# Performance work log

Measured on AMD Instinct MI355X. Metric: run time of the kernel, lower is better.

Reference implementation:

```python
import jax, jax.numpy as jnp
import numpy as np
import math

B, S, DM, DQ, DK, DV = 4, 4096, 512, 512, 512, 512
MASKED = True


def setup_inputs() -> dict:
    key = jax.random.key(0)
    ks = jax.random.split(key, 9)
    s = 1.0 / math.sqrt(DM)  # ~ torch Linear init scale
    return {
        "q_in": jax.random.normal(ks[0], (B, S, DM), jnp.float32),
        "k_in": jax.random.normal(ks[1], (B, S, DM), jnp.float32),
        "v_in": jax.random.normal(ks[2], (B, S, DM), jnp.float32),
        "Wq": jax.random.uniform(ks[3], (DQ, DM), jnp.float32, -s, s),
        "bq": jax.random.uniform(ks[4], (DQ,), jnp.float32, -s, s),
        "Wk": jax.random.uniform(ks[5], (DK, DM), jnp.float32, -s, s),
        "bk": jax.random.uniform(ks[6], (DK,), jnp.float32, -s, s),
        "Wv": jax.random.uniform(ks[7], (DV, DM), jnp.float32, -s, s),
        "bv": jax.random.uniform(ks[8], (DV,), jnp.float32, -s, s),
    }


def reference(q_in, k_in, v_in, Wq, bq, Wk, bk, Wv, bv):
    # Linear projections (torch Linear: x @ W.T + b)
    q = jnp.einsum("bsm,qm->bsq", q_in, Wq) + bq  # [B,S,DQ]
    k = jnp.einsum("bsm,km->bsk", k_in, Wk) + bk  # [B,S,DK]
    v = jnp.einsum("bsm,vm->bsv", v_in, Wv) + bv  # [B,S,DV]

    scale = 1.0 / math.sqrt(k.shape[-1])
    scores = jnp.einsum("bqd,bkd->bqk", q, k) * scale  # [B,S,S]
    if MASKED:
        # Faithful to torch.tril on the scores: upper triangle set to 0 (NOT -inf)
        tri = jnp.tril(jnp.ones((scores.shape[1], scores.shape[2]), bool))
        scores = jnp.where(tri, scores, jnp.zeros((), scores.dtype))
    attn = jax.nn.softmax(scores, axis=-1)
    return jnp.einsum("bqk,bkv->bqv", attn, v)  # [B,S,DV]
```

## Files before the change

### kernel.cpp

```cpp
#include <hip/hip_runtime.h>

typedef unsigned short u16;
typedef unsigned int   u32;
typedef __bf16  bf16x8 __attribute__((ext_vector_type(8)));
typedef u16     u16x8  __attribute__((ext_vector_type(8)));
typedef float   f32x4  __attribute__((ext_vector_type(4)));

#define S_LEN   4096
#define DMODEL  512
#define NBATCH  4
#define NTILE   32
#define NPAIR   528

__device__ __forceinline__ u16 f2bf(float x){
  u32 u = __float_as_uint(x);
  return (u16)((u + 0x7fffu + ((u >> 16) & 1u)) >> 16);
}
__device__ __forceinline__ float bf2f(u16 u){ return __uint_as_float(((u32)u) << 16); }

__device__ __forceinline__ void gload_lds16(const void* g, void* l){
  __builtin_amdgcn_global_load_lds((const __attribute__((address_space(1))) void*)g,
                                   (__attribute__((address_space(3))) void*)l, 16, 0, 0);
}

__device__ __forceinline__ bf16x8 ones_frag(){
  u16x8 u = {0x3F80,0x3F80,0x3F80,0x3F80,0x3F80,0x3F80,0x3F80,0x3F80};
  return __builtin_bit_cast(bf16x8, u);
}

__global__ __launch_bounds__(256) void cast_kernel(const float* __restrict__ in,
                                                   u16* __restrict__ out, int n8){
  int i = blockIdx.x * 256 + threadIdx.x;
  int stride = gridDim.x * 256;
  for (; i < n8; i += stride){
    const float4* p = (const float4*)in + (size_t)i * 2;
    float4 a = p[0], b = p[1];
    ushort4 o0 = make_ushort4(f2bf(a.x), f2bf(a.y), f2bf(a.z), f2bf(a.w));
    ushort4 o1 = make_ushort4(f2bf(b.x), f2bf(b.y), f2bf(b.z), f2bf(b.w));
    ((ushort4*)out)[(size_t)i*2]   = o0;
    ((ushort4*)out)[(size_t)i*2+1] = o1;
  }
}

template<bool ZS>
__device__ __forceinline__ void mma_step(const u16* __restrict__ A, int lda,
                                         const u16* __restrict__ B, int ldb,
                                         u16* ldsA, u16* ldsB,
                                         f32x4 acc[4][4], f32x4* accz, bf16x8 ones,
                                         int w, int l, int wr, int wc)
{
  int srow = l >> 2, scol = (l & 3) * 8;
  #pragma unroll
  for (int cc = 0; cc < 2; ++cc){
    int c = w + cc * 4;
    gload_lds16(A + (size_t)(c*16 + srow)*lda + scol, ldsA + c*512);
    gload_lds16(B + (size_t)(c*16 + srow)*ldb + scol, ldsB + c*512);
  }
  __syncthreads();
  int lo = l & 15, hi = l >> 4;
  bf16x8 a[4], b[4];
  #pragma unroll
  for (int m = 0; m < 4; m++) a[m] = *(const bf16x8*)(ldsA + (wr*64 + m*16 + lo)*32 + hi*8);
  #pragma unroll
  for (int n = 0; n < 4; n++) b[n] = *(const bf16x8*)(ldsB + (wc*64 + n*16 + lo)*32 + hi*8);
  #pragma unroll
  for (int m = 0; m < 4; m++){
    if constexpr (ZS)
      accz[m] = __builtin_amdgcn_mfma_f32_16x16x32_bf16(a[m], ones, accz[m], 0, 0, 0);
    #pragma unroll
    for (int n = 0; n < 4; n++)
      acc[m][n] = __builtin_amdgcn_mfma_f32_16x16x32_bf16(a[m], b[n], acc[m][n], 0, 0, 0);
  }
  __syncthreads();
}

__global__ __launch_bounds__(256) void proj_kernel(const u16* __restrict__ X,
                                                   const u16* __restrict__ W,
                                                   const float* __restrict__ bias,
                                                   u16* __restrict__ Y)
{
  __shared__ __align__(16) u16 ldsA[4096], ldsB[4096];
  int cn = blockIdx.x, rm = blockIdx.y;
  int t = threadIdx.x, w = t >> 6, l = t & 63, wr = w >> 1, wc = w & 1;
  f32x4 zero = {0.f,0.f,0.f,0.f};
  f32x4 acc[4][4];
  #pragma unroll
  for (int m = 0; m < 4; m++)
    #pragma unroll
    for (int n = 0; n < 4; n++) acc[m][n] = zero;

  const u16* A = X + (size_t)rm * 128 * DMODEL;
  const u16* B = W + (size_t)cn * 128 * DMODEL;
  for (int s = 0; s < 16; s++)
    mma_step<false>(A + s*32, DMODEL, B + s*32, DMODEL, ldsA, ldsB, acc, nullptr,
                    ones_frag(), w, l, wr, wc);

  int lo = l & 15, hi = l >> 4;
  #pragma unroll
  for (int n = 0; n < 4; n++){
    int col = cn*128 + wc*64 + n*16 + lo;
    float bs = bias[col];
    #pragma unroll
    for (int m = 0; m < 4; m++){
      int row0 = rm*128 + wr*64 + m*16 + hi*4;
      #pragma unroll
      for (int j = 0; j < 4; j++)
        Y[(size_t)(row0 + j) * DMODEL + col] = f2bf(acc[m][n][j] + bs);
    }
  }
}

__global__ __launch_bounds__(256) void transpose_kernel(const u16* __restrict__ V,
                                                        u16* __restrict__ Vt)
{
  __shared__ u16 tile[64][66];
  int k0 = blockIdx.x * 64, c0 = blockIdx.y * 64, b = blockIdx.z;
  int t = threadIdx.x;
  #pragma unroll
  for (int i = 0; i < 16; i++){
    int idx = i*256 + t; int r = idx >> 6, c = idx & 63;
    tile[r][c] = V[((size_t)b*S_LEN + k0 + r) * DMODEL + c0 + c];
  }
  __syncthreads();
  #pragma unroll
  for (int i = 0; i < 16; i++){
    int idx = i*256 + t; int r = idx >> 6, c = idx & 63;
    Vt[((size_t)b*DMODEL + c0 + r) * S_LEN + k0 + c] = tile[c][r];
  }
}

__global__ __launch_bounds__(256) void vpart_kernel(const u16* __restrict__ V,
                                                    float* __restrict__ part){
  int t = blockIdx.x, b = blockIdx.y, c = threadIdx.x;
  const u16* base = V + ((size_t)b*S_LEN + t*128) * DMODEL;
  float s0 = 0.f, s1 = 0.f;
  for (int k = 0; k < 128; k++){
    s0 += bf2f(base[(size_t)k*DMODEL + c]);
    s1 += bf2f(base[(size_t)k*DMODEL + 256 + c]);
  }
  part[((size_t)b*NTILE + t)*DMODEL + c]       = s0;
  part[((size_t)b*NTILE + t)*DMODEL + 256 + c] = s1;
}

__global__ void suffix_kernel(const float* __restrict__ part, float* __restrict__ sufx){
  int b = blockIdx.x, c = threadIdx.x;
  float s = 0.f;
  for (int t = NTILE - 1; t >= 0; t--){
    sufx[((size_t)b*NTILE + t)*DMODEL + c] = s;
    s += part[((size_t)b*NTILE + t)*DMODEL + c];
  }
}

__global__ __launch_bounds__(256) void score_kernel(const u16* __restrict__ Q,
                                                    const u16* __restrict__ K,
                                                    u16* __restrict__ P)
{
  __shared__ __align__(16) u16 ldsA[4096], ldsB[4096];
  int p = blockIdx.x, b = blockIdx.y;
  int qt = (int)((sqrtf(8.f*p + 1.f) - 1.f) * 0.5f);
  while ((qt+1)*(qt+2)/2 <= p) qt++;
  while (qt*(qt+1)/2 > p) qt--;
  int kt = p - qt*(qt+1)/2;

  int t = threadIdx.x, w = t >> 6, l = t & 63, wr = w >> 1, wc = w & 1;
  f32x4 zero = {0.f,0.f,0.f,0.f};
  f32x4 acc[4][4];
  #pragma unroll
  for (int m = 0; m < 4; m++)
    #pragma unroll
    for (int n = 0; n < 4; n++) acc[m][n] = zero;

  const u16* A = Q + ((size_t)b*S_LEN + qt*128) * DMODEL;
  const u16* B = K + ((size_t)b*S_LEN + kt*128) * DMODEL;
  for (int s = 0; s < 16; s++)
    mma_step<false>(A + s*32, DMODEL, B + s*32, DMODEL, ldsA, ldsB, acc, nullptr,
                    ones_frag(), w, l, wr, wc);

  const float scale = 0.044194173824159216f;
  u16* Pt = P + ((size_t)b*NPAIR + p) * 16384;
  int lo = l & 15, hi = l >> 4;
  bool diag = (qt == kt);
  #pragma unroll
  for (int m = 0; m < 4; m++){
    #pragma unroll
    for (int n = 0; n < 4; n++){
      int cl = wc*64 + n*16 + lo;
      #pragma unroll
      for (int j = 0; j < 4; j++){
        int rl = wr*64 + m*16 + hi*4 + j;
        float s = acc[m][n][j] * scale;
        if (diag && cl > rl) s = 0.f;
        Pt[(size_t)rl*128 + cl] = f2bf(__expf(s));
      }
    }
  }
}

__global__ __launch_bounds__(256) void pv_kernel(const u16* __restrict__ P,
                                                 const u16* __restrict__ Vt,
                                                 const float* __restrict__ sufx,
                                                 float* __restrict__ out)
{
  __shared__ __align__(16) u16 ldsA[4096], ldsB[4096];
  int ct = blockIdx.x, qt = (NTILE - 1) - blockIdx.y, b = blockIdx.z;
  int t = threadIdx.x, w = t >> 6, l = t & 63, wr = w >> 1, wc = w & 1;
  f32x4 zero = {0.f,0.f,0.f,0.f};
  f32x4 acc[4][4]; f32x4 accz[4];
  #pragma unroll
  for (int m = 0; m < 4; m++){
    accz[m] = zero;
    #pragma unroll
    for (int n = 0; n < 4; n++) acc[m][n] = zero;
  }
  bf16x8 ones = ones_frag();

  for (int kt = 0; kt <= qt; ++kt){
    const u16* A = P + ((size_t)b*NPAIR + qt*(qt+1)/2 + kt) * 16384;
    const u16* B = Vt + ((size_t)b*DMODEL + ct*128) * S_LEN + kt*128;
    #pragma unroll 1
    for (int s = 0; s < 4; s++)
      mma_step<true>(A + s*32, 128, B + s*32, S_LEN, ldsA, ldsB, acc, accz,
                     ones, w, l, wr, wc);
  }

  float zadd = (float)(S_LEN - (qt+1)*128);
  int lo = l & 15, hi = l >> 4;
  const float* suf = sufx + ((size_t)b*NTILE + qt)*DMODEL + ct*128;
  #pragma unroll
  for (int m = 0; m < 4; m++){
    #pragma unroll
    for (int j = 0; j < 4; j++){
      float Z = accz[m][j] + zadd;
      int rl = wr*64 + m*16 + hi*4 + j;
      #pragma unroll
      for (int n = 0; n < 4; n++){
        int cl = wc*64 + n*16 + lo;
        float o = (acc[m][n][j] + suf[cl]) / Z;
        out[((size_t)b*S_LEN + qt*128 + rl) * DMODEL + ct*128 + cl] = o;
      }
    }
  }
}

extern "C" void kernel_launch(void* const* d_in, const int* in_sizes, int n_in,
                              void* d_out, int out_size, void* d_ws, size_t ws_size,
                              hipStream_t stream)
{
  const float* q_in = (const float*)d_in[0];
  const float* k_in = (const float*)d_in[1];
  const float* v_in = (const float*)d_in[2];
  const float* Wq   = (const float*)d_in[3];
  const float* bq   = (const float*)d_in[4];
  const float* Wk   = (const float*)d_in[5];
  const float* bk   = (const float*)d_in[6];
  const float* Wv   = (const float*)d_in[7];
  const float* bv   = (const float*)d_in[8];
  float* out = (float*)d_out;
  char*  ws  = (char*)d_ws;

  const size_t NTOK  = (size_t)NBATCH * S_LEN;
  const size_t TEN_B = NTOK * DMODEL * 2;

  size_t off = 0;
  u16* Wq_b = (u16*)(ws + off); off += DMODEL*DMODEL*2;
  u16* Wk_b = (u16*)(ws + off); off += DMODEL*DMODEL*2;
  u16* Wv_b = (u16*)(ws + off); off += DMODEL*DMODEL*2;
  size_t uoff = off;
  u16* qx = (u16*)(ws + uoff);
  u16* kx = qx + NTOK*DMODEL;
  u16* vx = kx + NTOK*DMODEL;
  u16* Pbuf = (u16*)(ws + uoff);
  size_t usize = (size_t)NBATCH * NPAIR * 16384 * 2;
  off = uoff + usize;
  u16* Qb  = (u16*)(ws + off); off += TEN_B;
  u16* Kb  = (u16*)(ws + off); off += TEN_B;
  u16* Vb  = (u16*)(ws + off); off += TEN_B;
  u16* Vtb = (u16*)(ws + off); off += TEN_B;
  float* part = (float*)(ws + off); off += (size_t)NBATCH*NTILE*DMODEL*4;
  float* sufx = (float*)(ws + off); off += (size_t)NBATCH*NTILE*DMODEL*4;

  int n8_big = (int)(NTOK * DMODEL / 8);
  int n8_w   = DMODEL * DMODEL / 8;
  cast_kernel<<<2048, 256, 0, stream>>>(q_in, qx, n8_big);
  cast_kernel<<<2048, 256, 0, stream>>>(k_in, kx, n8_big);
  cast_kernel<<<2048, 256, 0, stream>>>(v_in, vx, n8_big);
  cast_kernel<<<128, 256, 0, stream>>>(Wq, Wq_b, n8_w);
  cast_kernel<<<128, 256, 0, stream>>>(Wk, Wk_b, n8_w);
  cast_kernel<<<128, 256, 0, stream>>>(Wv, Wv_b, n8_w);

  dim3 pg(DMODEL/128, (unsigned)(NTOK/128));
  proj_kernel<<<pg, 256, 0, stream>>>(qx, Wq_b, bq, Qb);
  proj_kernel<<<pg, 256, 0, stream>>>(kx, Wk_b, bk, Kb);
  proj_kernel<<<pg, 256, 0, stream>>>(vx, Wv_b, bv, Vb);

  transpose_kernel<<<dim3(S_LEN/64, DMODEL/64, NBATCH), 256, 0, stream>>>(Vb, Vtb);
  vpart_kernel<<<dim3(NTILE, NBATCH), 256, 0, stream>>>(Vb, part);
  suffix_kernel<<<NBATCH, DMODEL, 0, stream>>>(part, sufx);

  score_kernel<<<dim3(NPAIR, NBATCH), 256, 0, stream>>>(Qb, Kb, Pbuf);
  pv_kernel<<<dim3(DMODEL/128, NTILE, NBATCH), 256, 0, stream>>>(Pbuf, Vtb, sufx, out);
}
```

Before: 379.0 us.

## Retile score and PV kernels to single-wave 64x64 tiles with double-buffered LDS

Score and PV kernels move from 256-thread 128x128 tiles to 64-thread 64x64 tiles. Each uses a double-buffered LDS pipeline with explicit waitcnt, and block indices are remapped for XCD-aware scheduling. The softmax denominator is now built in the score kernel with shuffle reductions and atomics, which removes the extra ones-MFMA from PV. The three cast launches and the three projection launches are each merged into one grid. The smaller tiles give more blocks and better balance on the causal triangle, but each block gets less data reuse, and the atomics and a zeroing launch add overhead.

```diff
diff --git a/kernel.cpp b/kernel.cpp
--- a/kernel.cpp
+++ b/kernel.cpp
@@ -11,6 +11,7 @@
 #define NBATCH  4
 #define NTILE   32
 #define NPAIR   528
+#define SCALE   0.044194173824159216f
 
 __device__ __forceinline__ u16 f2bf(float x){
   u32 u = __float_as_uint(x);
@@ -23,79 +24,76 @@
                                    (__attribute__((address_space(3))) void*)l, 16, 0, 0);
 }
 
-__device__ __forceinline__ bf16x8 ones_frag(){
-  u16x8 u = {0x3F80,0x3F80,0x3F80,0x3F80,0x3F80,0x3F80,0x3F80,0x3F80};
-  return __builtin_bit_cast(bf16x8, u);
-}
-
-__global__ __launch_bounds__(256) void cast_kernel(const float* __restrict__ in,
-                                                   u16* __restrict__ out, int n8){
+__global__ __launch_bounds__(256) void cast3_kernel(const float* __restrict__ a,
+                                                    const float* __restrict__ b,
+                                                    const float* __restrict__ c,
+                                                    u16* oa, u16* ob, u16* oc, int n8){
+  int z = blockIdx.y;
+  const float* in = (z == 0) ? a : (z == 1) ? b : c;
+  u16* out = (z == 0) ? oa : (z == 1) ? ob : oc;
   int i = blockIdx.x * 256 + threadIdx.x;
   int stride = gridDim.x * 256;
   for (; i < n8; i += stride){
     const float4* p = (const float4*)in + (size_t)i * 2;
-    float4 a = p[0], b = p[1];
-    ushort4 o0 = make_ushort4(f2bf(a.x), f2bf(a.y), f2bf(a.z), f2bf(a.w));
-    ushort4 o1 = make_ushort4(f2bf(b.x), f2bf(b.y), f2bf(b.z), f2bf(b.w));
+    float4 x = p[0], y = p[1];
+    ushort4 o0 = make_ushort4(f2bf(x.x), f2bf(x.y), f2bf(x.z), f2bf(x.w));
+    ushort4 o1 = make_ushort4(f2bf(y.x), f2bf(y.y), f2bf(y.z), f2bf(y.w));
     ((ushort4*)out)[(size_t)i*2]   = o0;
     ((ushort4*)out)[(size_t)i*2+1] = o1;
   }
 }
 
-template<bool ZS>
-__device__ __forceinline__ void mma_step(const u16* __restrict__ A, int lda,
-                                         const u16* __restrict__ B, int ldb,
-                                         u16* ldsA, u16* ldsB,
-                                         f32x4 acc[4][4], f32x4* accz, bf16x8 ones,
-                                         int w, int l, int wr, int wc)
-{
-  int srow = l >> 2, scol = (l & 3) * 8;
-  #pragma unroll
-  for (int cc = 0; cc < 2; ++cc){
-    int c = w + cc * 4;
-    gload_lds16(A + (size_t)(c*16 + srow)*lda + scol, ldsA + c*512);
-    gload_lds16(B + (size_t)(c*16 + srow)*ldb + scol, ldsB + c*512);
-  }
-  __syncthreads();
-  int lo = l & 15, hi = l >> 4;
-  bf16x8 a[4], b[4];
-  #pragma unroll
-  for (int m = 0; m < 4; m++) a[m] = *(const bf16x8*)(ldsA + (wr*64 + m*16 + lo)*32 + hi*8);
-  #pragma unroll
-  for (int n = 0; n < 4; n++) b[n] = *(const bf16x8*)(ldsB + (wc*64 + n*16 + lo)*32 + hi*8);
-  #pragma unroll
-  for (int m = 0; m < 4; m++){
-    if constexpr (ZS)
-      accz[m] = __builtin_amdgcn_mfma_f32_16x16x32_bf16(a[m], ones, accz[m], 0, 0, 0);
-    #pragma unroll
-    for (int n = 0; n < 4; n++)
-      acc[m][n] = __builtin_amdgcn_mfma_f32_16x16x32_bf16(a[m], b[n], acc[m][n], 0, 0, 0);
-  }
-  __syncthreads();
-}
-
-__global__ __launch_bounds__(256) void proj_kernel(const u16* __restrict__ X,
-                                                   const u16* __restrict__ W,
-                                                   const float* __restrict__ bias,
-                                                   u16* __restrict__ Y)
+__global__ __launch_bounds__(256) void zero_kernel(float* __restrict__ p, int n){
+  int i = blockIdx.x * 256 + threadIdx.x;
+  if (i < n) p[i] = 0.f;
+}
+
+__global__ __launch_bounds__(256) void proj_kernel(
+    const u16* __restrict__ qx, const u16* __restrict__ kx, const u16* __restrict__ vx,
+    const u16* __restrict__ Wq, const u16* __restrict__ Wk, const u16* __restrict__ Wv,
+    const float* __restrict__ bq, const float* __restrict__ bk, const float* __restrict__ bv,
+    u16* Qb, u16* Kb, u16* Vb)
 {
   __shared__ __align__(16) u16 ldsA[4096], ldsB[4096];
+  int z = blockIdx.z;
+  const u16* X = (z==0) ? qx : (z==1) ? kx : vx;
+  const u16* W = (z==0) ? Wq : (z==1) ? Wk : Wv;
+  const float* bias = (z==0) ? bq : (z==1) ? bk : bv;
+  u16* Y = (z==0) ? Qb : (z==1) ? Kb : Vb;
+
   int cn = blockIdx.x, rm = blockIdx.y;
   int t = threadIdx.x, w = t >> 6, l = t & 63, wr = w >> 1, wc = w & 1;
-  f32x4 zero = {0.f,0.f,0.f,0.f};
   f32x4 acc[4][4];
   #pragma unroll
   for (int m = 0; m < 4; m++)
     #pragma unroll
-    for (int n = 0; n < 4; n++) acc[m][n] = zero;
+    for (int n = 0; n < 4; n++) acc[m][n] = (f32x4){0.f,0.f,0.f,0.f};
 
   const u16* A = X + (size_t)rm * 128 * DMODEL;
   const u16* B = W + (size_t)cn * 128 * DMODEL;
-  for (int s = 0; s < 16; s++)
-    mma_step<false>(A + s*32, DMODEL, B + s*32, DMODEL, ldsA, ldsB, acc, nullptr,
-                    ones_frag(), w, l, wr, wc);
-
+  int srow = l >> 2, scol = (l & 3) * 8;
   int lo = l & 15, hi = l >> 4;
+  for (int s = 0; s < 16; s++){
+    #pragma unroll
+    for (int cc = 0; cc < 2; ++cc){
+      int c = w + cc * 4;
+      gload_lds16(A + (size_t)(c*16 + srow)*DMODEL + s*32 + scol, ldsA + c*512);
+      gload_lds16(B + (size_t)(c*16 + srow)*DMODEL + s*32 + scol, ldsB + c*512);
+    }
+    __syncthreads();
+    bf16x8 fa[4], fb[4];
+    #pragma unroll
+    for (int m = 0; m < 4; m++) fa[m] = *(const bf16x8*)(ldsA + (wr*64 + m*16 + lo)*32 + hi*8);
+    #pragma unroll
+    for (int n = 0; n < 4; n++) fb[n] = *(const bf16x8*)(ldsB + (wc*64 + n*16 + lo)*32 + hi*8);
+    #pragma unroll
+    for (int m = 0; m < 4; m++)
+      #pragma unroll
+      for (int n = 0; n < 4; n++)
+        acc[m][n] = __builtin_amdgcn_mfma_f32_16x16x32_bf16(fa[m], fb[n], acc[m][n], 0, 0, 0);
+    __syncthreads();
+  }
+
   #pragma unroll
   for (int n = 0; n < 4; n++){
     int col = cn*128 + wc*64 + n*16 + lo;
@@ -151,92 +149,178 @@
   }
 }
 
-__global__ __launch_bounds__(256) void score_kernel(const u16* __restrict__ Q,
-                                                    const u16* __restrict__ K,
-                                                    u16* __restrict__ P)
-{
-  __shared__ __align__(16) u16 ldsA[4096], ldsB[4096];
-  int p = blockIdx.x, b = blockIdx.y;
-  int qt = (int)((sqrtf(8.f*p + 1.f) - 1.f) * 0.5f);
-  while ((qt+1)*(qt+2)/2 <= p) qt++;
-  while (qt*(qt+1)/2 > p) qt--;
-  int kt = p - qt*(qt+1)/2;
-
-  int t = threadIdx.x, w = t >> 6, l = t & 63, wr = w >> 1, wc = w & 1;
-  f32x4 zero = {0.f,0.f,0.f,0.f};
+__global__ __launch_bounds__(64) void score_kernel(const u16* __restrict__ Q,
+                                                   const u16* __restrict__ K,
+                                                   u16* __restrict__ P,
+                                                   float* __restrict__ Z)
+{
+  __shared__ __align__(16) u16 ldsA[2][2048], ldsB[2][2048];
+  int flat = blockIdx.x;
+  int w = (flat & 7) * 1056 + (flat >> 3);
+  int b = w / 2112, r = w % 2112;
+  int tp = (int)((sqrtf(1.f + 2.f*(float)r) - 1.f) * 0.5f);
+  while (2*(tp+1)*(tp+2) <= r) tp++;
+  while (2*tp*(tp+1) > r) tp--;
+  int rem = r - 2*tp*(tp+1);
+  int qi, ki;
+  if (rem < 2*tp + 2){ qi = 2*tp; ki = rem; } else { qi = 2*tp + 1; ki = rem - (2*tp + 2); }
+
+  int l = threadIdx.x;
+  int lr = l >> 2, lc = (l & 3) * 8;
+  int lo = l & 15, hi = l >> 4;
+
+  const u16* A = Q + ((size_t)b*S_LEN + (size_t)qi*64) * DMODEL;
+  const u16* B = K + ((size_t)b*S_LEN + (size_t)ki*64) * DMODEL;
+
   f32x4 acc[4][4];
   #pragma unroll
   for (int m = 0; m < 4; m++)
     #pragma unroll
-    for (int n = 0; n < 4; n++) acc[m][n] = zero;
-
-  const u16* A = Q + ((size_t)b*S_LEN + qt*128) * DMODEL;
-  const u16* B = K + ((size_t)b*S_LEN + kt*128) * DMODEL;
-  for (int s = 0; s < 16; s++)
-    mma_step<false>(A + s*32, DMODEL, B + s*32, DMODEL, ldsA, ldsB, acc, nullptr,
-                    ones_frag(), w, l, wr, wc);
-
-  const float scale = 0.044194173824159216f;
-  u16* Pt = P + ((size_t)b*NPAIR + p) * 16384;
+    for (int n = 0; n < 4; n++) acc[m][n] = (f32x4){0.f,0.f,0.f,0.f};
+
+#define SC_STAGE(tt, buf) { \
+    int s32 = (tt)*32; \
+    _Pragma("unroll") \
+    for (int c = 0; c < 4; c++){ \
+      gload_lds16(A + (size_t)(c*16 + lr)*DMODEL + s32 + lc, &ldsA[buf][c*512]); \
+      gload_lds16(B + (size_t)(c*16 + lr)*DMODEL + s32 + lc, &ldsB[buf][c*512]); \
+    } }
+
+  if (ki <= qi){
+    SC_STAGE(0, 0);
+    #pragma unroll 2
+    for (int tt = 0; tt < 16; ++tt){
+      int cur = tt & 1;
+      asm volatile("s_waitcnt lgkmcnt(0)" ::: "memory");
+      if (tt < 15){
+        SC_STAGE(tt + 1, cur ^ 1);
+        asm volatile("s_waitcnt vmcnt(8)" ::: "memory");
+      } else {
+        asm volatile("s_waitcnt vmcnt(0)" ::: "memory");
+      }
+      __builtin_amdgcn_sched_barrier(0);
+      bf16x8 fa[4], fb[4];
+      #pragma unroll
+      for (int m = 0; m < 4; m++) fa[m] = *(const bf16x8*)(&ldsA[cur][(m*16 + lo)*32 + hi*8]);
+      #pragma unroll
+      for (int n = 0; n < 4; n++) fb[n] = *(const bf16x8*)(&ldsB[cur][(n*16 + lo)*32 + hi*8]);
+      #pragma unroll
+      for (int m = 0; m < 4; m++)
+        #pragma unroll
+        for (int n = 0; n < 4; n++)
+          acc[m][n] = __builtin_amdgcn_mfma_f32_16x16x32_bf16(fa[m], fb[n], acc[m][n], 0, 0, 0);
+    }
+  }
+#undef SC_STAGE
+
+  int qt = qi >> 1, kt = ki >> 1;
+  u16* Pt = P + ((size_t)b*NPAIR + (size_t)qt*(qt+1)/2 + kt) * 16384
+              + (size_t)(qi & 1) * 64 * 128 + (size_t)(ki & 1) * 64;
+  #pragma unroll
+  for (int m = 0; m < 4; m++){
+    #pragma unroll
+    for (int j = 0; j < 4; j++){
+      int row = m*16 + hi*4 + j;
+      int grow = qi*64 + row;
+      float rsum = 0.f;
+      #pragma unroll
+      for (int n = 0; n < 4; n++){
+        int col = n*16 + lo;
+        int gcol = ki*64 + col;
+        float s = (gcol > grow) ? 0.f : acc[m][n][j] * SCALE;
+        u16 pb = f2bf(__expf(s));
+        Pt[(size_t)row*128 + col] = pb;
+        rsum += bf2f(pb);
+      }
+      rsum += __shfl_xor(rsum, 1);
+      rsum += __shfl_xor(rsum, 2);
+      rsum += __shfl_xor(rsum, 4);
+      rsum += __shfl_xor(rsum, 8);
+      if (lo == 0) atomicAdd(&Z[(size_t)b*S_LEN + grow], rsum);
+    }
+  }
+}
+
+__global__ __launch_bounds__(64) void pv_kernel(const u16* __restrict__ P,
+                                                const u16* __restrict__ Vt,
+                                                const float* __restrict__ sufx,
+                                                const float* __restrict__ Z,
+                                                float* __restrict__ out)
+{
+  __shared__ __align__(16) u16 ldsA[2][2048], ldsB[2][2048];
+  int flat = (blockIdx.z*64 + blockIdx.y)*8 + blockIdx.x;
+  int w = (flat & 7) * 256 + (flat >> 3);
+  int b  = w >> 9;
+  int qip = (w >> 3) & 63;
+  int qi  = (qip & 1) ? (qip >> 1) : 63 - (qip >> 1);
+  int ci  = w & 7;
+  int qt  = qi >> 1;
+
+  int l = threadIdx.x;
+  int lr = l >> 2, lc = (l & 3) * 8;
   int lo = l & 15, hi = l >> 4;
-  bool diag = (qt == kt);
+
+  const u16* Abase = P + ((size_t)b*NPAIR + (size_t)qt*(qt+1)/2) * 16384
+                       + (size_t)(qi & 1) * 64 * 128;
+  const u16* Bbase = Vt + ((size_t)b*DMODEL + (size_t)ci*64) * S_LEN;
+
+  f32x4 acc[4][4];
+  #pragma unroll
+  for (int m = 0; m < 4; m++)
+    #pragma unroll
+    for (int n = 0; n < 4; n++) acc[m][n] = (f32x4){0.f,0.f,0.f,0.f};
+
+  int nstep = (qt + 1) * 4;
+
+#define PV_STAGE(tt, buf) { \
+    int kt_ = (tt) >> 2, s_ = ((tt) & 3) * 32; \
+    const u16* A_ = Abase + (size_t)kt_*16384 + s_; \
+    const u16* B_ = Bbase + kt_*128 + s_; \
+    _Pragma("unroll") \
+    for (int c = 0; c < 4; c++){ \
+      gload_lds16(A_ + (size_t)(c*16 + lr)*128 + lc, &ldsA[buf][c*512]); \
+      gload_lds16(B_ + (size_t)(c*16 + lr)*S_LEN + lc, &ldsB[buf][c*512]); \
+    } }
+
+  PV_STAGE(0, 0);
+  #pragma unroll 2
+  for (int tt = 0; tt < nstep; ++tt){
+    int cur = tt & 1;
+    asm volatile("s_waitcnt lgkmcnt(0)" ::: "memory");
+    if (tt + 1 < nstep){
+      PV_STAGE(tt + 1, cur ^ 1);
+      asm volatile("s_waitcnt vmcnt(8)" ::: "memory");
+    } else {
+      asm volatile("s_waitcnt vmcnt(0)" ::: "memory");
+    }
+    __builtin_amdgcn_sched_barrier(0);
+    bf16x8 fa[4], fb[4];
+    #pragma unroll
+    for (int m = 0; m < 4; m++) fa[m] = *(const bf16x8*)(&ldsA[cur][(m*16 + lo)*32 + hi*8]);
+    #pragma unroll
+    for (int n = 0; n < 4; n++) fb[n] = *(const bf16x8*)(&ldsB[cur][(n*16 + lo)*32 + hi*8]);
+    #pragma unroll
+    for (int m = 0; m < 4; m++)
+      #pragma unroll
+      for (int n = 0; n < 4; n++)
+        acc[m][n] = __builtin_amdgcn_mfma_f32_16x16x32_bf16(fa[m], fb[n], acc[m][n], 0, 0, 0);
+  }
+#undef PV_STAGE
+
+  float zadd = (float)(S_LEN - (qt + 1) * 128);
+  const float* suf = sufx + ((size_t)b*NTILE + qt)*DMODEL + ci*64;
+  const float* Zp  = Z + (size_t)b*S_LEN + (size_t)qi*64;
+  float* O = out + ((size_t)b*S_LEN + (size_t)qi*64) * DMODEL + ci*64;
   #pragma unroll
   for (int m = 0; m < 4; m++){
     #pragma unroll
-    for (int n = 0; n < 4; n++){
-      int cl = wc*64 + n*16 + lo;
-      #pragma unroll
-      for (int j = 0; j < 4; j++){
-        int rl = wr*64 + m*16 + hi*4 + j;
-        float s = acc[m][n][j] * scale;
-        if (diag && cl > rl) s = 0.f;
-        Pt[(size_t)rl*128 + cl] = f2bf(__expf(s));
-      }
-    }
-  }
-}
-
-__global__ __launch_bounds__(256) void pv_kernel(const u16* __restrict__ P,
-                                                 const u16* __restrict__ Vt,
-                                                 const float* __restrict__ sufx,
-                                                 float* __restrict__ out)
-{
-  __shared__ __align__(16) u16 ldsA[4096], ldsB[4096];
-  int ct = blockIdx.x, qt = (NTILE - 1) - blockIdx.y, b = blockIdx.z;
-  int t = threadIdx.x, w = t >> 6, l = t & 63, wr = w >> 1, wc = w & 1;
-  f32x4 zero = {0.f,0.f,0.f,0.f};
-  f32x4 acc[4][4]; f32x4 accz[4];
-  #pragma unroll
-  for (int m = 0; m < 4; m++){
-    accz[m] = zero;
-    #pragma unroll
-    for (int n = 0; n < 4; n++) acc[m][n] = zero;
-  }
-  bf16x8 ones = ones_frag();
-
-  for (int kt = 0; kt <= qt; ++kt){
-    const u16* A = P + ((size_t)b*NPAIR + qt*(qt+1)/2 + kt) * 16384;
-    const u16* B = Vt + ((size_t)b*DMODEL + ct*128) * S_LEN + kt*128;
-    #pragma unroll 1
-    for (int s = 0; s < 4; s++)
-      mma_step<true>(A + s*32, 128, B + s*32, S_LEN, ldsA, ldsB, acc, accz,
-                     ones, w, l, wr, wc);
-  }
-
-  float zadd = (float)(S_LEN - (qt+1)*128);
-  int lo = l & 15, hi = l >> 4;
-  const float* suf = sufx + ((size_t)b*NTILE + qt)*DMODEL + ct*128;
-  #pragma unroll
-  for (int m = 0; m < 4; m++){
-    #pragma unroll
     for (int j = 0; j < 4; j++){
-      float Z = accz[m][j] + zadd;
-      int rl = wr*64 + m*16 + hi*4 + j;
+      int row = m*16 + hi*4 + j;
+      float rz = 1.f / (Zp[row] + zadd);
       #pragma unroll
       for (int n = 0; n < 4; n++){
-        int cl = wc*64 + n*16 + lo;
-        float o = (acc[m][n][j] + suf[cl]) / Z;
-        out[((size_t)b*S_LEN + qt*128 + rl) * DMODEL + ct*128 + cl] = o;
+        int col = n*16 + lo;
+        O[(size_t)row*DMODEL + col] = (acc[m][n][j] + suf[col]) * rz;
       }
     }
   }
@@ -278,25 +362,21 @@
   u16* Vtb = (u16*)(ws + off); off += TEN_B;
   float* part = (float*)(ws + off); off += (size_t)NBATCH*NTILE*DMODEL*4;
   float* sufx = (float*)(ws + off); off += (size_t)NBATCH*NTILE*DMODEL*4;
+  float* Zful = (float*)(ws + off); off += (size_t)NBATCH*S_LEN*4;
 
   int n8_big = (int)(NTOK * DMODEL / 8);
   int n8_w   = DMODEL * DMODEL / 8;
-  cast_kernel<<<2048, 256, 0, stream>>>(q_in, qx, n8_big);
-  cast_kernel<<<2048, 256, 0, stream>>>(k_in, kx, n8_big);
-  cast_kernel<<<2048, 256, 0, stream>>>(v_in, vx, n8_big);
-  cast_kernel<<<128, 256, 0, stream>>>(Wq, Wq_b, n8_w);
-  cast_kernel<<<128, 256, 0, stream>>>(Wk, Wk_b, n8_w);
-  cast_kernel<<<128, 256, 0, stream>>>(Wv, Wv_b, n8_w);
-
-  dim3 pg(DMODEL/128, (unsigned)(NTOK/128));
-  proj_kernel<<<pg, 256, 0, stream>>>(qx, Wq_b, bq, Qb);
-  proj_kernel<<<pg, 256, 0, stream>>>(kx, Wk_b, bk, Kb);
-  proj_kernel<<<pg, 256, 0, stream>>>(vx, Wv_b, bv, Vb);
+  cast3_kernel<<<dim3(2048, 3), 256, 0, stream>>>(q_in, k_in, v_in, qx, kx, vx, n8_big);
+  cast3_kernel<<<dim3(128, 3), 256, 0, stream>>>(Wq, Wk, Wv, Wq_b, Wk_b, Wv_b, n8_w);
+  zero_kernel<<<(NBATCH*S_LEN + 255)/256, 256, 0, stream>>>(Zful, NBATCH*S_LEN);
+
+  proj_kernel<<<dim3(DMODEL/128, (unsigned)(NTOK/128), 3), 256, 0, stream>>>(
+      qx, kx, vx, Wq_b, Wk_b, Wv_b, bq, bk, bv, Qb, Kb, Vb);
 
   transpose_kernel<<<dim3(S_LEN/64, DMODEL/64, NBATCH), 256, 0, stream>>>(Vb, Vtb);
   vpart_kernel<<<dim3(NTILE, NBATCH), 256, 0, stream>>>(Vb, part);
   suffix_kernel<<<NBATCH, DMODEL, 0, stream>>>(part, sufx);
 
-  score_kernel<<<dim3(NPAIR, NBATCH), 256, 0, stream>>>(Qb, Kb, Pbuf);
-  pv_kernel<<<dim3(DMODEL/128, NTILE, NBATCH), 256, 0, stream>>>(Pbuf, Vtb, sufx, out);
-}
+  score_kernel<<<8448, 64, 0, stream>>>(Qb, Kb, Pbuf, Zful);
+  pv_kernel<<<dim3(8, 64, NBATCH), 64, 0, stream>>>(Pbuf, Vtb, sufx, Zful, out);
+}
```

New measurement: 399.2 us. 5.3% more time.
